# Optimization experiments

Hardware: AMD Instinct MI355X
Metric: run time of the kernel (lower is better)

The kernel has to match this reference:

```python
import jax, jax.numpy as jnp
import numpy as np

HIDDEN = 256
NH = 8
D = HIDDEN // NH
TP = (2.0 * D) ** 0.5  # temperature = sqrt(temperature_coeff * head_dim)


def setup_inputs() -> dict:
    key = jax.random.key(0)
    ks = jax.random.split(key, 6)
    n_b, n_a = 16, 512
    x = jax.random.normal(ks[0], (n_b, n_a, HIDDEN), dtype=jnp.float32)
    mask = jax.random.randint(ks[1], (1, n_b, n_a, n_a), 0, 2) == 1  # bool, True = masked
    adjacency_matrix = jax.random.normal(ks[2], (1, n_b, n_a, n_a), dtype=jnp.float32)
    scale = 1.0 / np.sqrt(HIDDEN)
    Wq = jax.random.normal(ks[3], (HIDDEN, HIDDEN), dtype=jnp.float32) * scale
    Wk = jax.random.normal(ks[4], (HIDDEN, HIDDEN), dtype=jnp.float32) * scale
    Wv = jax.random.normal(ks[5], (HIDDEN, HIDDEN), dtype=jnp.float32) * scale
    return {"x": x, "mask": mask, "adjacency_matrix": adjacency_matrix,
            "Wq": Wq, "Wk": Wk, "Wv": Wv}


def reference(x, mask, adjacency_matrix, Wq, Wk, Wv):
    n_b, n_a, _ = x.shape
    # nn.Linear(bias=False): y = x @ W^T ; split into heads, head dim leading
    q = (x @ Wq.T).reshape(n_b, n_a, NH, D)
    k = (x @ Wk.T).reshape(n_b, n_a, NH, D)
    v = (x @ Wv.T).reshape(n_b, n_a, NH, D)
    # scores: (nh, n_b, n_a, n_a); adjacency (1,n_b,n_a,n_a) broadcasts over heads
    a = jnp.einsum("bqhd,bkhd->hbqk", q, k) / TP + adjacency_matrix
    a = jnp.where(mask, -jnp.inf, a)
    alpha = jax.nn.softmax(a, axis=-1)
    attn = jnp.einsum("hbqk,bkhd->bqhd", alpha, v).reshape(n_b, n_a, HIDDEN)
    return attn + x
```

## Files before the change

### kernel.cpp

```cpp
#include <hip/hip_runtime.h>
#include <hip/hip_bf16.h>


#define NB 16
#define NA 512
#define HID 256
#define NHEAD 8
#define DH 32
#define INV_TP 0.125f
#define ADJ_LD 520

typedef __attribute__((ext_vector_type(8))) short short8;
typedef __attribute__((ext_vector_type(4))) float floatx4;

__device__ __forceinline__ unsigned short f2bf(float f) {
  unsigned int u = __builtin_bit_cast(unsigned int, f);
  u += 0x7fffu + ((u >> 16) & 1u);
  return (unsigned short)(u >> 16);
}

__device__ __forceinline__ floatx4 mfma16(short8 a, short8 b, floatx4 c) {
  return __builtin_amdgcn_mfma_f32_16x16x32_bf16(a, b, c, 0, 0, 0);
}

__device__ __forceinline__ short8 ld8f32_bf16(const float* __restrict__ p) {
  float4 a = *(const float4*)p;
  float4 b = *(const float4*)(p + 4);
  short8 r;
  r[0] = (short)f2bf(a.x); r[1] = (short)f2bf(a.y);
  r[2] = (short)f2bf(a.z); r[3] = (short)f2bf(a.w);
  r[4] = (short)f2bf(b.x); r[5] = (short)f2bf(b.y);
  r[6] = (short)f2bf(b.z); r[7] = (short)f2bf(b.w);
  return r;
}

__device__ __forceinline__ int vperm32(int g) {
  return (((g & 15) >> 2) << 3) + (g & 3) + (((g >> 4) & 1) << 2);
}

__global__ __launch_bounds__(256) void cvt_bf16(
    const float* __restrict__ X, const float* __restrict__ Wq,
    const float* __restrict__ Wk, const float* __restrict__ Wv,
    unsigned short* __restrict__ Xbf, unsigned short* __restrict__ Wbf) {
  const int tid = blockIdx.x * blockDim.x + threadIdx.x;
  const int stride = gridDim.x * blockDim.x;
  for (int i = tid; i < (NB * NA * HID) / 4; i += stride) {
    float4 v = ((const float4*)X)[i];
    ushort4 w;
    w.x = f2bf(v.x); w.y = f2bf(v.y); w.z = f2bf(v.z); w.w = f2bf(v.w);
    ((ushort4*)Xbf)[i] = w;
  }
  for (int i = tid; i < (HID * HID) / 4; i += stride) {
    float4 v = ((const float4*)Wq)[i];
    ushort4 w;
    w.x = f2bf(v.x); w.y = f2bf(v.y); w.z = f2bf(v.z); w.w = f2bf(v.w);
    ((ushort4*)Wbf)[i] = w;
    v = ((const float4*)Wk)[i];
    w.x = f2bf(v.x); w.y = f2bf(v.y); w.z = f2bf(v.z); w.w = f2bf(v.w);
    ((ushort4*)(Wbf + HID * HID))[i] = w;
    v = ((const float4*)Wv)[i];
    w.x = f2bf(v.x); w.y = f2bf(v.y); w.z = f2bf(v.z); w.w = f2bf(v.w);
    ((ushort4*)(Wbf + 2 * HID * HID))[i] = w;
  }
}

__global__ __launch_bounds__(256) void qkv_proj_bf(
    const unsigned short* __restrict__ Xbf, const unsigned short* __restrict__ Wbf,
    unsigned short* __restrict__ Y) {
  const unsigned short* W = Wbf + (size_t)blockIdx.y * (HID * HID);
  unsigned short* Yo = Y + (size_t)blockIdx.y * (NB * NHEAD * NA * DH);
  const int wave = threadIdx.x >> 6, lane = threadIdx.x & 63;
  const int lr = lane & 15, lh = lane >> 4;
  const int m0 = blockIdx.x * 32;
  const int cb = wave * 64;
  const floatx4 z = {0.f, 0.f, 0.f, 0.f};
  floatx4 acc[2][4];
#pragma unroll
  for (int i = 0; i < 2; i++)
#pragma unroll
    for (int j = 0; j < 4; j++) acc[i][j] = z;

  for (int kb = 0; kb < HID; kb += 32) {
    short8 a[2], bw[4];
#pragma unroll
    for (int rt = 0; rt < 2; rt++)
      a[rt] = *(const short8*)&Xbf[(size_t)(m0 + rt * 16 + lr) * HID + kb + lh * 8];
#pragma unroll
    for (int ci = 0; ci < 4; ci++)
      bw[ci] = *(const short8*)&W[(size_t)(cb + ci * 16 + lr) * HID + kb + lh * 8];
#pragma unroll
    for (int rt = 0; rt < 2; rt++)
#pragma unroll
      for (int ci = 0; ci < 4; ci++)
        acc[rt][ci] = mfma16(a[rt], bw[ci], acc[rt][ci]);
  }
  if (blockIdx.y == 2) {
#pragma unroll
    for (int rt = 0; rt < 2; rt++)
#pragma unroll
      for (int ci = 0; ci < 4; ci++) {
        int m = m0 + rt * 16 + lh * 4;
        int c = cb + ci * 16 + lr;
        int bb = m >> 9, n0 = m & 511, hh = c >> 5, dd = c & 31;
        int np = (n0 & ~31) | vperm32(n0 & 31);
        ushort4 w;
        w.x = f2bf(acc[rt][ci][0]);
        w.y = f2bf(acc[rt][ci][1]);
        w.z = f2bf(acc[rt][ci][2]);
        w.w = f2bf(acc[rt][ci][3]);
        *(ushort4*)&Yo[((size_t)(bb * NHEAD + hh) * DH + dd) * NA + np] = w;
      }
  } else {
#pragma unroll
    for (int rt = 0; rt < 2; rt++)
#pragma unroll
      for (int ci = 0; ci < 4; ci++)
#pragma unroll
        for (int r = 0; r < 4; r++) {
          int m = m0 + rt * 16 + lh * 4 + r;
          int c = cb + ci * 16 + lr;
          int bb = m >> 9, n = m & 511, hh = c >> 5, dd = c & 31;
          Yo[((size_t)(bb * NHEAD + hh) * NA + n) * DH + dd] = f2bf(acc[rt][ci][r]);
        }
  }
}

__global__ __launch_bounds__(256) void qkv_proj(
    const float* __restrict__ X, const float* __restrict__ Wq,
    const float* __restrict__ Wk, const float* __restrict__ Wv,
    unsigned short* __restrict__ Y) {
  const float* W = (blockIdx.y == 0) ? Wq : (blockIdx.y == 1) ? Wk : Wv;
  unsigned short* Yo = Y + (size_t)blockIdx.y * (NB * NHEAD * NA * DH);
  const int wave = threadIdx.x >> 6, lane = threadIdx.x & 63;
  const int lr = lane & 15, lh = lane >> 4;
  const int m0 = blockIdx.x * 32;
  const int cb = wave * 64;
  const floatx4 z = {0.f, 0.f, 0.f, 0.f};
  floatx4 acc[2][4];
#pragma unroll
  for (int i = 0; i < 2; i++)
#pragma unroll
    for (int j = 0; j < 4; j++) acc[i][j] = z;

  for (int kb = 0; kb < HID; kb += 32) {
    short8 a[2], bw[4];
#pragma unroll
    for (int rt = 0; rt < 2; rt++)
      a[rt] = ld8f32_bf16(X + (size_t)(m0 + rt * 16 + lr) * HID + kb + lh * 8);
#pragma unroll
    for (int ci = 0; ci < 4; ci++)
      bw[ci] = ld8f32_bf16(W + (size_t)(cb + ci * 16 + lr) * HID + kb + lh * 8);
#pragma unroll
    for (int rt = 0; rt < 2; rt++)
#pragma unroll
      for (int ci = 0; ci < 4; ci++)
        acc[rt][ci] = mfma16(a[rt], bw[ci], acc[rt][ci]);
  }
  if (blockIdx.y == 2) {
#pragma unroll
    for (int rt = 0; rt < 2; rt++)
#pragma unroll
      for (int ci = 0; ci < 4; ci++) {
        int m = m0 + rt * 16 + lh * 4;
        int c = cb + ci * 16 + lr;
        int bb = m >> 9, n0 = m & 511, hh = c >> 5, dd = c & 31;
        int np = (n0 & ~31) | vperm32(n0 & 31);
        ushort4 w;
        w.x = f2bf(acc[rt][ci][0]);
        w.y = f2bf(acc[rt][ci][1]);
        w.z = f2bf(acc[rt][ci][2]);
        w.w = f2bf(acc[rt][ci][3]);
        *(ushort4*)&Yo[((size_t)(bb * NHEAD + hh) * DH + dd) * NA + np] = w;
      }
  } else {
#pragma unroll
    for (int rt = 0; rt < 2; rt++)
#pragma unroll
      for (int ci = 0; ci < 4; ci++)
#pragma unroll
        for (int r = 0; r < 4; r++) {
          int m = m0 + rt * 16 + lh * 4 + r;
          int c = cb + ci * 16 + lr;
          int bb = m >> 9, n = m & 511, hh = c >> 5, dd = c & 31;
          Yo[((size_t)(bb * NHEAD + hh) * NA + n) * DH + dd] = f2bf(acc[rt][ci][r]);
        }
  }
}

__global__ __launch_bounds__(512, 2) void attn_fused(
    const unsigned short* __restrict__ Qw, const unsigned short* __restrict__ Kw,
    const unsigned short* __restrict__ Vtg, const float* __restrict__ X,
    const unsigned char* __restrict__ maskB, const int* __restrict__ maskI,
    const float* __restrict__ adj, float* __restrict__ out) {
  __shared__ float adj_lds[16][ADJ_LD];
  const int qb = blockIdx.x, b = blockIdx.y;
  const int t = threadIdx.x;
  const int h = t >> 6, lane = t & 63, lr = lane & 15, lh = lane >> 4;
  const int q0 = qb * 16;
  const size_t bh = (size_t)(b * NHEAD + h) * NA * DH;
  const unsigned short* Kg = Kw + bh;
  const unsigned short* Vg = Vtg + bh;

  short8 qf = *(const short8*)&Qw[bh + (size_t)(q0 + lr) * DH + lh * 8];
  short8 kf[8];
#pragma unroll
  for (int kt = 0; kt < 8; kt++)
    kf[kt] = *(const short8*)&Kg[(size_t)(kt * 16 + lr) * DH + lh * 8];

  const unsigned int* mu = (const unsigned int*)maskB;
  unsigned int cnt = 0;
#pragma unroll
  for (int j = 0; j < 8; j++) cnt += (mu[lane + j * 64] != 0u) ? 1u : 0u;
#pragma unroll
  for (int off = 32; off > 0; off >>= 1) cnt += __shfl_xor(cnt, off);
  const bool mBytes = (cnt > 368u);

#pragma unroll
  for (int j = 0; j < 4; j++) {
    const int slot = t + j * 512;
    const int srow = slot >> 7;
    const int sc4 = (slot & 127) * 4;
    const size_t soff = ((size_t)b * NA + q0 + srow) * NA + sc4;
    float4 av = *(const float4*)&adj[soff];
    if (mBytes) {
      uchar4 mb = *(const uchar4*)&maskB[soff];
      if (mb.x) av.x = -1e30f;
      if (mb.y) av.y = -1e30f;
      if (mb.z) av.z = -1e30f;
      if (mb.w) av.w = -1e30f;
    } else {
      int4 mi = *(const int4*)&maskI[soff];
      if (mi.x) av.x = -1e30f;
      if (mi.y) av.y = -1e30f;
      if (mi.z) av.z = -1e30f;
      if (mi.w) av.w = -1e30f;
    }
    *(float4*)&adj_lds[srow][sc4] = av;
  }
  __syncthreads();

  const floatx4 z = {0.f, 0.f, 0.f, 0.f};
  float m_run = -3.0e38f, l_run = 0.f;
  floatx4 o0 = z, o1 = z;

#pragma unroll 1
  for (int tile = 0; tile < 4; ++tile) {
    const int keyoff = tile * 128;

    short8 vf0[4], vf1[4];
#pragma unroll
    for (int kc = 0; kc < 4; kc++) {
      const int kbase = keyoff + kc * 32 + lh * 8;
      vf0[kc] = *(const short8*)&Vg[(size_t)lr * NA + kbase];
      vf1[kc] = *(const short8*)&Vg[(size_t)(16 + lr) * NA + kbase];
    }
    __builtin_amdgcn_sched_barrier(0);

    floatx4 s[8];
#pragma unroll
    for (int kt = 0; kt < 8; kt++) s[kt] = z;
#pragma unroll
    for (int kt = 0; kt < 8; kt++) s[kt] = mfma16(kf[kt], qf, s[kt]);

    if (tile < 3) {
      const int nko = keyoff + 128;
#pragma unroll
      for (int kt = 0; kt < 8; kt++)
        kf[kt] = *(const short8*)&Kg[(size_t)(nko + kt * 16 + lr) * DH + lh * 8];
    }
    __builtin_amdgcn_sched_barrier(0);

    float pmax = -3.0e38f;
#pragma unroll
    for (int kt = 0; kt < 8; kt++) {
      float4 av = *(const float4*)&adj_lds[lr][keyoff + kt * 16 + lh * 4];
      float v0 = s[kt][0] * INV_TP + av.x;
      float v1 = s[kt][1] * INV_TP + av.y;
      float v2 = s[kt][2] * INV_TP + av.z;
      float v3 = s[kt][3] * INV_TP + av.w;
      s[kt][0] = v0; s[kt][1] = v1; s[kt][2] = v2; s[kt][3] = v3;
      pmax = fmaxf(pmax, fmaxf(fmaxf(v0, v1), fmaxf(v2, v3)));
    }
    pmax = fmaxf(pmax, __shfl_xor(pmax, 16));
    pmax = fmaxf(pmax, __shfl_xor(pmax, 32));

    const float mnew = fmaxf(m_run, pmax);
    if (tile) {
      const float corr = __expf(m_run - mnew);
      l_run *= corr;
#pragma unroll
      for (int r = 0; r < 4; r++) {
        float c = __shfl(corr, lh * 4 + r, 64);
        o0[r] *= c;
        o1[r] *= c;
      }
    }
    m_run = mnew;

    float sum = 0.f;
#pragma unroll
    for (int kt = 0; kt < 8; kt++) {
      float e0 = __expf(s[kt][0] - mnew);
      float e1 = __expf(s[kt][1] - mnew);
      float e2 = __expf(s[kt][2] - mnew);
      float e3 = __expf(s[kt][3] - mnew);
      s[kt][0] = e0; s[kt][1] = e1; s[kt][2] = e2; s[kt][3] = e3;
      sum += (e0 + e1) + (e2 + e3);
    }
    sum += __shfl_xor(sum, 16);
    sum += __shfl_xor(sum, 32);
    l_run += sum;

#pragma unroll
    for (int kc = 0; kc < 4; kc++) {
      union { short8 s8; unsigned int u[4]; } aa;
      aa.u[0] = (unsigned int)f2bf(s[2 * kc][0]) |
                ((unsigned int)f2bf(s[2 * kc][1]) << 16);
      aa.u[1] = (unsigned int)f2bf(s[2 * kc][2]) |
                ((unsigned int)f2bf(s[2 * kc][3]) << 16);
      aa.u[2] = (unsigned int)f2bf(s[2 * kc + 1][0]) |
                ((unsigned int)f2bf(s[2 * kc + 1][1]) << 16);
      aa.u[3] = (unsigned int)f2bf(s[2 * kc + 1][2]) |
                ((unsigned int)f2bf(s[2 * kc + 1][3]) << 16);
      o0 = mfma16(aa.s8, vf0[kc], o0);
      o1 = mfma16(aa.s8, vf1[kc], o1);
    }
  }

  const float inv = 1.0f / l_run;
#pragma unroll
  for (int r = 0; r < 4; r++) {
    float iv = __shfl(inv, lh * 4 + r, 64);
    size_t idx = ((size_t)b * NA + (q0 + lh * 4 + r)) * HID + h * DH + lr;
    out[idx] = o0[r] * iv + X[idx];
    out[idx + 16] = o1[r] * iv + X[idx + 16];
  }
}

extern "C" void kernel_launch(void* const* d_in, const int* in_sizes, int n_in,
                              void* d_out, int out_size, void* d_ws, size_t ws_size,
                              hipStream_t stream) {
  const float* x = (const float*)d_in[0];
  const void* mask = d_in[1];
  const float* adj = (const float*)d_in[2];
  const float* Wq = (const float*)d_in[3];
  const float* Wk = (const float*)d_in[4];
  const float* Wv = (const float*)d_in[5];
  float* out = (float*)d_out;

  char* ws = (char*)d_ws;
  const size_t MB = 1048576;
  const size_t NEED = 4 * MB + 512 * 1024 + 3 * 4 * MB;

  unsigned short *Qw, *Kw, *Vw;
  if (ws_size >= NEED) {
    unsigned short* Xbf = (unsigned short*)ws;
    unsigned short* Wbf = (unsigned short*)(ws + 4 * MB);
    Qw = (unsigned short*)(ws + 4 * MB + 512 * 1024);
    Kw = (unsigned short*)(ws + 8 * MB + 512 * 1024);
    Vw = (unsigned short*)(ws + 12 * MB + 512 * 1024);
    cvt_bf16<<<1024, 256, 0, stream>>>(x, Wq, Wk, Wv, Xbf, Wbf);
    qkv_proj_bf<<<dim3(256, 3), 256, 0, stream>>>(Xbf, Wbf, Qw);
  } else {
    Qw = (unsigned short*)(ws + 4096);
    Kw = (unsigned short*)(ws + 4096 + 4 * MB);
    Vw = (unsigned short*)(ws + 4096 + 8 * MB);
    qkv_proj<<<dim3(256, 3), 256, 0, stream>>>(x, Wq, Wk, Wv, Qw);
  }
  attn_fused<<<dim3(32, NB), 512, 0, stream>>>(
      Qw, Kw, Vw, x, (const unsigned char*)mask, (const int*)mask, adj, out);
}
```

Before: 60.95 us.

## Fuse X bf16 conversion into QKV projection and stage stores through LDS

The separate pass that converted X to bf16 in global memory is removed. Each projection block now loads its 32 fp32 rows of X, converts them and keeps them in shared memory as the MFMA A operand, and only the weights are still converted by a small kernel. The Q/K output is written through shared memory as coalesced 16-byte rows instead of scattered 2-byte stores. This cuts an 8MB write plus reads of the intermediate and shrinks the pre-pass, but X is re-read and re-converted by each of the three projection blocks per row tile, and extra barriers are added.

```diff
diff --git a/kernel.cpp b/kernel.cpp
--- a/kernel.cpp
+++ b/kernel.cpp
@@ -9,6 +9,7 @@
 #define DH 32
 #define INV_TP 0.125f
 #define ADJ_LD 520
+#define XT_LD 264
 
 typedef __attribute__((ext_vector_type(8))) short short8;
 typedef __attribute__((ext_vector_type(4))) float floatx4;
@@ -38,18 +39,11 @@
   return (((g & 15) >> 2) << 3) + (g & 3) + (((g >> 4) & 1) << 2);
 }
 
-__global__ __launch_bounds__(256) void cvt_bf16(
-    const float* __restrict__ X, const float* __restrict__ Wq,
-    const float* __restrict__ Wk, const float* __restrict__ Wv,
-    unsigned short* __restrict__ Xbf, unsigned short* __restrict__ Wbf) {
+__global__ __launch_bounds__(256) void cvt_w(
+    const float* __restrict__ Wq, const float* __restrict__ Wk,
+    const float* __restrict__ Wv, unsigned short* __restrict__ Wbf) {
   const int tid = blockIdx.x * blockDim.x + threadIdx.x;
   const int stride = gridDim.x * blockDim.x;
-  for (int i = tid; i < (NB * NA * HID) / 4; i += stride) {
-    float4 v = ((const float4*)X)[i];
-    ushort4 w;
-    w.x = f2bf(v.x); w.y = f2bf(v.y); w.z = f2bf(v.z); w.w = f2bf(v.w);
-    ((ushort4*)Xbf)[i] = w;
-  }
   for (int i = tid; i < (HID * HID) / 4; i += stride) {
     float4 v = ((const float4*)Wq)[i];
     ushort4 w;
@@ -64,15 +58,31 @@
   }
 }
 
-__global__ __launch_bounds__(256) void qkv_proj_bf(
-    const unsigned short* __restrict__ Xbf, const unsigned short* __restrict__ Wbf,
+__global__ __launch_bounds__(256) void qkv_fused(
+    const float* __restrict__ X, const unsigned short* __restrict__ Wbf,
     unsigned short* __restrict__ Y) {
+  __shared__ __align__(16) unsigned short xt[32][XT_LD];
   const unsigned short* W = Wbf + (size_t)blockIdx.y * (HID * HID);
   unsigned short* Yo = Y + (size_t)blockIdx.y * (NB * NHEAD * NA * DH);
-  const int wave = threadIdx.x >> 6, lane = threadIdx.x & 63;
+  const int t = threadIdx.x;
+  const int wave = t >> 6, lane = t & 63;
   const int lr = lane & 15, lh = lane >> 4;
   const int m0 = blockIdx.x * 32;
   const int cb = wave * 64;
+
+  {
+    const int r = t >> 3, c0 = (t & 7) * 32;
+    const float* xrow = X + (size_t)(m0 + r) * HID + c0;
+#pragma unroll
+    for (int j = 0; j < 8; j++) {
+      float4 v = ((const float4*)xrow)[j];
+      ushort4 w;
+      w.x = f2bf(v.x); w.y = f2bf(v.y); w.z = f2bf(v.z); w.w = f2bf(v.w);
+      *(ushort4*)&xt[r][c0 + j * 4] = w;
+    }
+  }
+  __syncthreads();
+
   const floatx4 z = {0.f, 0.f, 0.f, 0.f};
   floatx4 acc[2][4];
 #pragma unroll
@@ -84,7 +94,7 @@
     short8 a[2], bw[4];
 #pragma unroll
     for (int rt = 0; rt < 2; rt++)
-      a[rt] = *(const short8*)&Xbf[(size_t)(m0 + rt * 16 + lr) * HID + kb + lh * 8];
+      a[rt] = *(const short8*)&xt[rt * 16 + lr][kb + lh * 8];
 #pragma unroll
     for (int ci = 0; ci < 4; ci++)
       bw[ci] = *(const short8*)&W[(size_t)(cb + ci * 16 + lr) * HID + kb + lh * 8];
@@ -94,6 +104,8 @@
       for (int ci = 0; ci < 4; ci++)
         acc[rt][ci] = mfma16(a[rt], bw[ci], acc[rt][ci]);
   }
+  __syncthreads();
+
   if (blockIdx.y == 2) {
 #pragma unroll
     for (int rt = 0; rt < 2; rt++)
@@ -110,18 +122,26 @@
         w.w = f2bf(acc[rt][ci][3]);
         *(ushort4*)&Yo[((size_t)(bb * NHEAD + hh) * DH + dd) * NA + np] = w;
       }
+    __syncthreads();
   } else {
 #pragma unroll
     for (int rt = 0; rt < 2; rt++)
 #pragma unroll
       for (int ci = 0; ci < 4; ci++)
 #pragma unroll
-        for (int r = 0; r < 4; r++) {
-          int m = m0 + rt * 16 + lh * 4 + r;
-          int c = cb + ci * 16 + lr;
-          int bb = m >> 9, n = m & 511, hh = c >> 5, dd = c & 31;
-          Yo[((size_t)(bb * NHEAD + hh) * NA + n) * DH + dd] = f2bf(acc[rt][ci][r]);
-        }
+        for (int r = 0; r < 4; r++)
+          xt[rt * 16 + lh * 4 + r][cb + ci * 16 + lr] = f2bf(acc[rt][ci][r]);
+    __syncthreads();
+#pragma unroll
+    for (int j = 0; j < 4; j++) {
+      const int chunk = t + j * 256;
+      const int row = chunk >> 5;
+      const int c0 = (chunk & 31) * 8;
+      const int n = m0 + row;
+      const int bb = n >> 9, nn = n & 511, hh = c0 >> 5, dd = c0 & 31;
+      *(uint4*)&Yo[((size_t)(bb * NHEAD + hh) * NA + nn) * DH + dd] =
+          *(const uint4*)&xt[row][c0];
+    }
   }
 }
 
@@ -350,17 +370,16 @@
 
   char* ws = (char*)d_ws;
   const size_t MB = 1048576;
-  const size_t NEED = 4 * MB + 512 * 1024 + 3 * 4 * MB;
+  const size_t NEED = 512 * 1024 + 3 * 4 * MB;
 
   unsigned short *Qw, *Kw, *Vw;
   if (ws_size >= NEED) {
-    unsigned short* Xbf = (unsigned short*)ws;
-    unsigned short* Wbf = (unsigned short*)(ws + 4 * MB);
-    Qw = (unsigned short*)(ws + 4 * MB + 512 * 1024);
-    Kw = (unsigned short*)(ws + 8 * MB + 512 * 1024);
-    Vw = (unsigned short*)(ws + 12 * MB + 512 * 1024);
-    cvt_bf16<<<1024, 256, 0, stream>>>(x, Wq, Wk, Wv, Xbf, Wbf);
-    qkv_proj_bf<<<dim3(256, 3), 256, 0, stream>>>(Xbf, Wbf, Qw);
+    unsigned short* Wbf = (unsigned short*)ws;
+    Qw = (unsigned short*)(ws + 512 * 1024);
+    Kw = (unsigned short*)(ws + 512 * 1024 + 4 * MB);
+    Vw = (unsigned short*)(ws + 512 * 1024 + 8 * MB);
+    cvt_w<<<64, 256, 0, stream>>>(Wq, Wk, Wv, Wbf);
+    qkv_fused<<<dim3(256, 3), 256, 0, stream>>>(x, Wbf, Qw);
   } else {
     Qw = (unsigned short*)(ws + 4096);
     Kw = (unsigned short*)(ws + 4096 + 4 * MB);
```

Result: faster. 58.38 us (-4.2%).
